# Kernel optimization log

Measured on AMD Instinct MI355X. Metric: run time of the kernel, lower is better.

Reference implementation:

```python
import jax, jax.numpy as jnp
import numpy as np

ALPHA = 0.2  # LeakyReLU negative slope
NEG_INF = -1.0e12


def setup_inputs() -> dict:
    key = jax.random.key(0)
    ks = jax.random.split(key, 8)
    N, F, D, H, M, Q = 4096, 512, 64, 4, 2, 128
    x = jax.random.normal(ks[0], (N, F), dtype=jnp.float32)
    adj = jax.random.randint(ks[1], (M, N, N), 0, 2, dtype=jnp.int32)
    W = jax.random.normal(ks[2], (H, F, D), dtype=jnp.float32) * 0.07
    a1 = jax.random.normal(ks[3], (H, D), dtype=jnp.float32) * 0.15
    a2 = jax.random.normal(ks[4], (H, D), dtype=jnp.float32) * 0.15
    Ws = jax.random.normal(ks[5], (H * D, Q), dtype=jnp.float32) * 0.1
    bs = jax.random.normal(ks[6], (1, Q), dtype=jnp.float32) * 0.1
    q_sem = jax.random.normal(ks[7], (Q, 1), dtype=jnp.float32) * 0.15
    return {"x": x, "adj": adj, "W": W, "a1": a1, "a2": a2,
            "Ws": Ws, "bs": bs, "q_sem": q_sem}


def reference(x, adj, W, a1, a2, Ws, bs, q_sem):
    N = x.shape[0]
    # Wh is identical across meta-paths (dropout disabled / eval mode)
    Wh = jnp.einsum('nf,hfd->hnd', x, W)            # [H,N,D]
    s1 = jnp.einsum('hnd,hd->hn', Wh, a1)           # Wh @ a[:D]
    s2 = jnp.einsum('hnd,hd->hn', Wh, a2)           # Wh @ a[D:]

    def metapath(adj_m):
        # e[h,i,j] = leaky_relu(s1[h,i] + s2[h,j]); mask by adjacency
        e = jax.nn.leaky_relu(s1[:, :, None] + s2[:, None, :], negative_slope=ALPHA)
        e = jnp.where(adj_m[None, :, :] > 0, e, NEG_INF)
        att = jax.nn.softmax(e, axis=2)             # softmax over neighbors (dim=1 in torch [N,N])
        h = jax.nn.elu(jnp.einsum('hnm,hmd->hnd', att, Wh))
        return jnp.transpose(h, (1, 0, 2)).reshape(N, -1)  # concat heads -> [N, H*D]

    Z = jax.vmap(metapath)(adj)                     # [M, N, H*D]
    z = jnp.transpose(Z, (1, 0, 2))                 # [N, M, H*D]

    # Semantic attention (faithful to original, incl. softmax over dim=1 of [M,1])
    Whs = jnp.tanh(jnp.einsum('nmf,fq->nmq', z, Ws) + bs)   # [N,M,Q]
    w = jnp.einsum('nmq,qo->nmo', Whs, q_sem).mean(0)        # [M,1]
    beta = jax.nn.softmax(w, axis=1)                          # [M,1]
    return (beta[None, :, :] * z).sum(axis=1)                 # [N, H*D]
```

## Files before the change

kernel.cpp:

```cpp
#include <hip/hip_runtime.h>
#include <hip/hip_fp16.h>
#include <stdint.h>

#define NN 4096
#define FF 512
#define DD 64
#define HH 4
#define MM 2
#define LOG2E 1.44269504088896340736f
#define ALPHA_LR 0.2f

typedef float f32x4 __attribute__((ext_vector_type(4)));
typedef _Float16 f16x8 __attribute__((ext_vector_type(8)));
typedef _Float16 f16x2 __attribute__((ext_vector_type(2)));
typedef unsigned short u16x2 __attribute__((ext_vector_type(2)));

extern "C" __device__ _Float16 __ocml_exp2_f16(_Float16);

union H4 { ushort4 u; _Float16 h[4]; };
union W8 { f16x8 v; uint32_t w[4]; f16x2 p[4]; };

__device__ inline float fast_exp2(float x) { return __builtin_amdgcn_exp2f(x); }
__device__ inline float fast_rcp(float x) { return __builtin_amdgcn_rcpf(x); }
__device__ inline f32x4 mfma16(f16x8 a, f16x8 b, f32x4 c) {
    return __builtin_amdgcn_mfma_f32_16x16x32_f16(a, b, c, 0, 0, 0);
}
__device__ inline uint32_t enc_f32(float f) {
    uint32_t u = __float_as_uint(f);
    return (u & 0x80000000u) ? ~u : (u | 0x80000000u);
}
__device__ inline float dec_f32(uint32_t k) {
    uint32_t u = (k & 0x80000000u) ? (k ^ 0x80000000u) : ~k;
    return __uint_as_float(u);
}
__device__ inline f16x2 msk01(uint32_t V, int k) {
    uint32_t w = (V >> (2 * k)) & 0x00010001u;
    u16x2 m = __builtin_bit_cast(u16x2, w) * (u16x2){0x3C00, 0x3C00};
    return __builtin_bit_cast(f16x2, m);
}
__device__ inline f16x2 pkmax(f16x2 a, f16x2 b) {
#if __has_builtin(__builtin_elementwise_max)
    return __builtin_elementwise_max(a, b);
#else
    return (f16x2){a[0] > b[0] ? a[0] : b[0], a[1] > b[1] ? a[1] : b[1]};
#endif
}

__global__ __launch_bounds__(256) void k_prep(const float* __restrict__ x,
                                              const int* __restrict__ adj,
                                              const float* __restrict__ W,
                                              _Float16* __restrict__ xh,
                                              _Float16* __restrict__ wt,
                                              unsigned long long* __restrict__ bitsT,
                                              uint32_t* __restrict__ m4a) {
    const int bid = blockIdx.x;
    if (bid < 2048) {
        const long long total = (long long)MM * NN * NN;
        const long long stride = 2048LL * 256;
        long long tid = (long long)bid * 256 + threadIdx.x;
        for (long long e = tid; e < total; e += stride) {
            unsigned long long msk = __ballot(adj[e] != 0);
            if ((threadIdx.x & 63) == 0) {
                long long q = e >> 6;
                int m  = (int)(q >> 18);
                int rem = (int)(q & 262143);
                int i  = rem >> 6;
                int jw = rem & 63;
                bitsT[((size_t)m * 64 + jw) * NN + i] = msk;
            }
        }
    } else if (bid < 4096) {
        int t = (bid - 2048) * 256 + threadIdx.x;
        if (t < HH) m4a[t] = 0u;
        float4 v = ((const float4*)x)[t];
        H4 o;
        o.h[0] = (_Float16)v.x; o.h[1] = (_Float16)v.y;
        o.h[2] = (_Float16)v.z; o.h[3] = (_Float16)v.w;
        ((ushort4*)xh)[t] = o.u;
    } else {
        int t = (bid - 4096) * 256 + threadIdx.x;
        int c = t >> 9, f = t & 511;
        int h = c >> 6, d = c & 63;
        wt[t] = (_Float16)W[(h * FF + f) * DD + d];
    }
}

__global__ __launch_bounds__(512) void k_wh(const _Float16* __restrict__ xh,
                                            const _Float16* __restrict__ wt,
                                            const float* __restrict__ a1,
                                            const float* __restrict__ a2,
                                            _Float16* __restrict__ whT,
                                            float* __restrict__ s1L,
                                            _Float16* __restrict__ s2h,
                                            uint32_t* __restrict__ m4a) {
    __shared__ float sred[8][2][16];
    const int wave = threadIdx.x >> 6;
    const int h    = wave & 3;
    const int th   = wave >> 2;
    const int lane = threadIdx.x & 63;
    const int iL   = lane & 15;
    const int quad = lane >> 4;
    const int i0   = blockIdx.x * 16;

    f32x4 acc[2];
    acc[0] = (f32x4){0.f, 0.f, 0.f, 0.f};
    acc[1] = (f32x4){0.f, 0.f, 0.f, 0.f};

    const _Float16* arow  = xh + (size_t)(i0 + iL) * FF + quad * 8;
    const _Float16* bbase = wt + (size_t)(h * 64 + th * 32 + iL) * FF + quad * 8;

    for (int kc = 0; kc < FF; kc += 32) {
        f16x8 a = *(const f16x8*)(arow + kc);
        #pragma unroll
        for (int u = 0; u < 2; ++u) {
            f16x8 b = *(const f16x8*)(bbase + (size_t)(16 * u) * FF + kc);
            acc[u] = mfma16(a, b, acc[u]);
        }
    }
    #pragma unroll
    for (int u = 0; u < 2; ++u) {
        H4 o;
        #pragma unroll
        for (int r = 0; r < 4; ++r) o.h[r] = (_Float16)acc[u][r];
        *(ushort4*)(whT + (size_t)(h * 64 + th * 32 + 16 * u + iL) * NN + i0 + quad * 4) = o.u;
    }

    const float a1v0 = a1[h * 64 + th * 32 + iL];
    const float a1v1 = a1[h * 64 + th * 32 + 16 + iL];
    const float a2v0 = a2[h * 64 + th * 32 + iL];
    const float a2v1 = a2[h * 64 + th * 32 + 16 + iL];
    #pragma unroll
    for (int r = 0; r < 4; ++r) {
        float p1 = acc[0][r] * a1v0 + acc[1][r] * a1v1;
        float p2 = acc[0][r] * a2v0 + acc[1][r] * a2v1;
        #pragma unroll
        for (int off = 1; off < 16; off <<= 1) {
            p1 += __shfl_xor(p1, off);
            p2 += __shfl_xor(p2, off);
        }
        if (iL == 0) {
            sred[wave][0][quad * 4 + r] = p1;
            sred[wave][1][quad * 4 + r] = p2;
        }
    }
    __syncthreads();
    if (threadIdx.x < 64) {
        int h2  = threadIdx.x >> 4;
        int idx = threadIdx.x & 15;
        float s1 = sred[h2][0][idx] + sred[h2 + 4][0][idx];
        float s2 = sred[h2][1][idx] + sred[h2 + 4][1][idx];
        float s2l = s2 * LOG2E;
        s1L[h2 * NN + i0 + idx] = s1 * LOG2E;
        s2h[h2 * NN + i0 + idx] = (_Float16)s2l;
        float mx = s2l;
        #pragma unroll
        for (int off = 1; off < 16; off <<= 1) mx = fmaxf(mx, __shfl_xor(mx, off));
        if (idx == 0) atomicMax(m4a + h2, enc_f32(mx));
    }
}

__global__ __launch_bounds__(512, 2) void k_attn(const _Float16* __restrict__ whT,
                                                 const float* __restrict__ s1L,
                                                 const _Float16* __restrict__ s2h,
                                                 const uint32_t* __restrict__ m4a,
                                                 const unsigned long long* __restrict__ bitsT,
                                                 float* __restrict__ out) {
    __shared__ __align__(16) float xr[8][MM][4][16][16];
    __shared__ __align__(16) float dr[8][MM][16];

    const int tid  = threadIdx.x;
    const int wave = tid >> 6;
    const int lane = tid & 63;
    const int iL   = lane & 15;
    const int quad = lane >> 4;
    const int h    = blockIdx.x & 3;
    const int i0   = (blockIdx.x >> 2) * 64;

    const float m4 = dec_f32(m4a[h]);
    f16x2 A2[4], B2[4];
    #pragma unroll
    for (int s = 0; s < 4; ++s) {
        float s1i = s1L[h * NN + i0 + 16 * s + iL];
        float vv  = s1i + m4;
        float cii = fmaxf(vv, ALPHA_LR * vv);
        _Float16 a = (_Float16)(s1i - cii);
        _Float16 b = (_Float16)(ALPHA_LR * s1i - cii);
        A2[s] = (f16x2){a, a};
        B2[s] = (f16x2){b, b};
    }
    const f16x2 al2 = (f16x2){(_Float16)ALPHA_LR, (_Float16)ALPHA_LR};

    f32x4 acc[4][MM][4];
    f32x4 accD[4][MM];
    #pragma unroll
    for (int s = 0; s < 4; ++s)
        #pragma unroll
        for (int m = 0; m < MM; ++m) {
            accD[s][m] = (f32x4){0.f, 0.f, 0.f, 0.f};
            #pragma unroll
            for (int t = 0; t < 4; ++t) acc[s][m][t] = (f32x4){0.f, 0.f, 0.f, 0.f};
        }

    f16x8 bones;
    #pragma unroll
    for (int e = 0; e < 8; ++e) bones[e] = (_Float16)1.0f;

    const _Float16* s2row = s2h + h * NN;
    const _Float16* brow = whT + (size_t)(h * 64 + iL) * NN;
    const int qshift = quad * 8;
    const int jbase = wave * 512;

    const unsigned long long* pB[MM][4];
    #pragma unroll
    for (int m = 0; m < MM; ++m)
        #pragma unroll
        for (int s = 0; s < 4; ++s)
            pB[m][s] = bitsT + (size_t)m * 64 * NN + i0 + 16 * s + iL;

    for (int it = 0; it < 8; ++it) {
        const int jc = jbase + it * 64;
        const int jw = jc >> 6;
        unsigned long long bm[MM][4];
        #pragma unroll
        for (int m = 0; m < MM; ++m)
            #pragma unroll
            for (int s = 0; s < 4; ++s)
                bm[m][s] = pB[m][s][(size_t)jw * NN];

        #pragma unroll
        for (int half = 0; half < 2; ++half) {
            const int jb = jc + 32 * half;
            f16x8 bfr[4];
            #pragma unroll
            for (int t = 0; t < 4; ++t)
                bfr[t] = *(const f16x8*)(brow + (size_t)(16 * t) * NN + jb + qshift);

            const W8 s2v = *(const W8*)(s2row + jb + qshift);
            const int shft = 32 * half + qshift;

            #pragma unroll
            for (int s = 0; s < 4; ++s) {
                uint32_t rs0 = (uint32_t)(bm[0][s] >> shft) & 0xFFu;
                uint32_t rs1 = (uint32_t)(bm[1][s] >> shft) & 0xFFu;
                uint32_t V0 = rs0 | (rs0 << 15);
                uint32_t V1 = rs1 | (rs1 << 15);
                W8 a0, a1v;
                #pragma unroll
                for (int k = 0; k < 4; ++k) {
                    f16x2 z = s2v.p[k] + A2[s];
                    f16x2 l = al2 * s2v.p[k] + B2[s];
                    f16x2 mx = pkmax(z, l);
                    f16x2 p = (f16x2){__ocml_exp2_f16(mx[0]), __ocml_exp2_f16(mx[1])};
                    a0.p[k]  = p * msk01(V0, k);
                    a1v.p[k] = p * msk01(V1, k);
                }
                #pragma unroll
                for (int t = 0; t < 4; ++t) {
                    acc[s][0][t] = mfma16(a0.v, bfr[t], acc[s][0][t]);
                    acc[s][1][t] = mfma16(a1v.v, bfr[t], acc[s][1][t]);
                }
                accD[s][0] = mfma16(a0.v, bones, accD[s][0]);
                accD[s][1] = mfma16(a1v.v, bones, accD[s][1]);
            }
        }
    }

    for (int s = 0; s < 4; ++s) {
        __syncthreads();
        #pragma unroll
        for (int m = 0; m < MM; ++m) {
            #pragma unroll
            for (int t = 0; t < 4; ++t)
                *(f32x4*)&xr[wave][m][t][iL][quad * 4] = acc[s][m][t];
            if (iL == 0) *(f32x4*)&dr[wave][m][quad * 4] = accD[s][m];
        }
        __syncthreads();
        if (wave < 4) {
            const int t = wave;
            f32x4 n0 = (f32x4){0.f, 0.f, 0.f, 0.f};
            f32x4 n1 = (f32x4){0.f, 0.f, 0.f, 0.f};
            f32x4 d0 = (f32x4){0.f, 0.f, 0.f, 0.f};
            f32x4 d1 = (f32x4){0.f, 0.f, 0.f, 0.f};
            #pragma unroll
            for (int sl = 0; sl < 8; ++sl) {
                n0 += *(const f32x4*)&xr[sl][0][t][iL][quad * 4];
                n1 += *(const f32x4*)&xr[sl][1][t][iL][quad * 4];
                d0 += *(const f32x4*)&dr[sl][0][quad * 4];
                d1 += *(const f32x4*)&dr[sl][1][quad * 4];
            }
            const int i0s = i0 + 16 * s;
            #pragma unroll
            for (int r = 0; r < 4; ++r) {
                float v0 = n0[r] * fast_rcp(d0[r]);
                float v1 = n1[r] * fast_rcp(d1[r]);
                float e0 = v0 > 0.f ? v0 : (fast_exp2(v0 * LOG2E) - 1.f);
                float e1 = v1 > 0.f ? v1 : (fast_exp2(v1 * LOG2E) - 1.f);
                out[(size_t)(i0s + quad * 4 + r) * (HH * DD) + h * 64 + 16 * t + iL] = e0 + e1;
            }
        }
    }
}

extern "C" void kernel_launch(void* const* d_in, const int* in_sizes, int n_in,
                              void* d_out, int out_size, void* d_ws, size_t ws_size,
                              hipStream_t stream) {
    const float* x   = (const float*)d_in[0];
    const int*   adj = (const int*)d_in[1];
    const float* W   = (const float*)d_in[2];
    const float* a1  = (const float*)d_in[3];
    const float* a2  = (const float*)d_in[4];
    float* out = (float*)d_out;

    char* ws = (char*)d_ws;
    _Float16* xh   = (_Float16*)(ws);
    _Float16* wt   = (_Float16*)(ws + 4194304);
    _Float16* whT  = (_Float16*)(ws + 4456448);
    float*    s1L  = (float*)(ws + 6553600);
    _Float16* s2h  = (_Float16*)(ws + 6619136);
    uint32_t* m4a  = (uint32_t*)(ws + 6684672);
    unsigned long long* bitsT = (unsigned long long*)(ws + 6750208);

    hipLaunchKernelGGL(k_prep, dim3(4608), dim3(256), 0, stream,
                       x, adj, W, xh, wt, bitsT, m4a);
    hipLaunchKernelGGL(k_wh, dim3(256), dim3(512), 0, stream,
                       xh, wt, a1, a2, whT, s1L, s2h, m4a);
    hipLaunchKernelGGL(k_attn, dim3(256), dim3(512), 0, stream,
                       whT, s1L, s2h, m4a, bitsT, out);
}
```

Before: 266.2 us.

## Restructure adjacency bit-packing, fuse x fp16 conversion into Wh GEMM, prefetch mask words

The adjacency packing now gives each block a 512-row by 64-column tile. Each wave issues 16 independent loads before its ballots, stages the masks in shared memory and writes them out as coalesced 128-bit stores, replacing scattered 8-byte stores. The separate x-to-fp16 conversion pass and its workspace buffer are removed; k_wh reads fp32 x directly and converts in registers. The attention kernel double-buffers the bitmask loads so the next iteration's mask words are fetched while the current one computes. The main risks are higher register pressure and the fp32 x being re-read by several blocks in k_wh.

```diff
diff --git a/kernel.cpp b/kernel.cpp
--- a/kernel.cpp
+++ b/kernel.cpp
@@ -46,46 +46,51 @@
 #endif
 }
 
-__global__ __launch_bounds__(256) void k_prep(const float* __restrict__ x,
-                                              const int* __restrict__ adj,
+__global__ __launch_bounds__(256) void k_prep(const int* __restrict__ adj,
                                               const float* __restrict__ W,
-                                              _Float16* __restrict__ xh,
                                               _Float16* __restrict__ wt,
                                               unsigned long long* __restrict__ bitsT,
                                               uint32_t* __restrict__ m4a) {
     const int bid = blockIdx.x;
-    if (bid < 2048) {
-        const long long total = (long long)MM * NN * NN;
-        const long long stride = 2048LL * 256;
-        long long tid = (long long)bid * 256 + threadIdx.x;
-        for (long long e = tid; e < total; e += stride) {
-            unsigned long long msk = __ballot(adj[e] != 0);
-            if ((threadIdx.x & 63) == 0) {
-                long long q = e >> 6;
-                int m  = (int)(q >> 18);
-                int rem = (int)(q & 262143);
-                int i  = rem >> 6;
-                int jw = rem & 63;
-                bitsT[((size_t)m * 64 + jw) * NN + i] = msk;
+    if (bid < 1024) {
+        __shared__ unsigned long long sw[512];
+        const int iq = bid & 7;
+        const int jw = (bid >> 3) & 63;
+        const int m  = bid >> 9;
+        const int w  = threadIdx.x >> 6;
+        const int l  = threadIdx.x & 63;
+        const int i0 = iq << 9;
+        const int* rp = adj + ((size_t)m << 24) + ((size_t)(i0 + (w << 7)) << 12)
+                        + (jw << 6) + l;
+        for (int t0 = 0; t0 < 128; t0 += 16) {
+            int v[16];
+            #pragma unroll
+            for (int u = 0; u < 16; ++u) v[u] = rp[(size_t)(t0 + u) << 12];
+            #pragma unroll
+            for (int u = 0; u < 16; ++u) {
+                unsigned long long msk = __ballot(v[u] != 0);
+                if (l == 0) sw[(w << 7) + t0 + u] = msk;
             }
         }
-    } else if (bid < 4096) {
-        int t = (bid - 2048) * 256 + threadIdx.x;
+        __syncthreads();
+        {
+            const int k = threadIdx.x;
+            unsigned long long* dst = bitsT + (((size_t)m * 64 + jw) << 12) + i0 + 2 * k;
+            ulonglong2 val;
+            val.x = sw[2 * k];
+            val.y = sw[2 * k + 1];
+            *(ulonglong2*)dst = val;
+        }
+    } else {
+        int t = (bid - 1024) * 256 + threadIdx.x;
         if (t < HH) m4a[t] = 0u;
-        float4 v = ((const float4*)x)[t];
-        H4 o;
-        o.h[0] = (_Float16)v.x; o.h[1] = (_Float16)v.y;
-        o.h[2] = (_Float16)v.z; o.h[3] = (_Float16)v.w;
-        ((ushort4*)xh)[t] = o.u;
-    } else {
-        int t = (bid - 4096) * 256 + threadIdx.x;
         int c = t >> 9, f = t & 511;
         int h = c >> 6, d = c & 63;
         wt[t] = (_Float16)W[(h * FF + f) * DD + d];
     }
 }
 
-__global__ __launch_bounds__(512) void k_wh(const _Float16* __restrict__ xh,
+__global__ __launch_bounds__(512) void k_wh(const float* __restrict__ x,
                                             const _Float16* __restrict__ wt,
                                             const float* __restrict__ a1,
                                             const float* __restrict__ a2,
@@ -106,11 +111,18 @@
     acc[0] = (f32x4){0.f, 0.f, 0.f, 0.f};
     acc[1] = (f32x4){0.f, 0.f, 0.f, 0.f};
 
-    const _Float16* arow  = xh + (size_t)(i0 + iL) * FF + quad * 8;
+    const float* arow = x + (size_t)(i0 + iL) * FF + quad * 8;
     const _Float16* bbase = wt + (size_t)(h * 64 + th * 32 + iL) * FF + quad * 8;
 
     for (int kc = 0; kc < FF; kc += 32) {
-        f16x8 a = *(const f16x8*)(arow + kc);
+        f32x4 xa = *(const f32x4*)(arow + kc);
+        f32x4 xb = *(const f32x4*)(arow + kc + 4);
+        f16x8 a;
+        #pragma unroll
+        for (int r = 0; r < 4; ++r) {
+            a[r]     = (_Float16)xa[r];
+            a[4 + r] = (_Float16)xb[r];
+        }
         #pragma unroll
         for (int u = 0; u < 2; ++u) {
             f16x8 b = *(const f16x8*)(bbase + (size_t)(16 * u) * FF + kc);
@@ -217,16 +229,17 @@
         for (int s = 0; s < 4; ++s)
             pB[m][s] = bitsT + (size_t)m * 64 * NN + i0 + 16 * s + iL;
 
-    for (int it = 0; it < 8; ++it) {
-        const int jc = jbase + it * 64;
-        const int jw = jc >> 6;
-        unsigned long long bm[MM][4];
+    auto loadB = [&](unsigned long long (&bm)[MM][4], int it) {
+        const int jw = (jbase + it * 64) >> 6;
         #pragma unroll
         for (int m = 0; m < MM; ++m)
             #pragma unroll
             for (int s = 0; s < 4; ++s)
                 bm[m][s] = pB[m][s][(size_t)jw * NN];
-
+    };
+
+    auto proc = [&](const unsigned long long (&bm)[MM][4], int it) {
+        const int jc = jbase + it * 64;
         #pragma unroll
         for (int half = 0; half < 2; ++half) {
             const int jb = jc + 32 * half;
@@ -263,6 +276,16 @@
                 accD[s][1] = mfma16(a1v.v, bones, accD[s][1]);
             }
         }
+    };
+
+    unsigned long long bmA[MM][4], bmB[MM][4];
+    loadB(bmA, 0);
+    #pragma unroll 1
+    for (int it = 0; it < 8; it += 2) {
+        loadB(bmB, it + 1);
+        proc(bmA, it);
+        if (it + 2 < 8) loadB(bmA, it + 2);
+        proc(bmB, it + 1);
     }
 
     for (int s = 0; s < 4; ++s) {
@@ -312,18 +335,17 @@
     float* out = (float*)d_out;
 
     char* ws = (char*)d_ws;
-    _Float16* xh   = (_Float16*)(ws);
-    _Float16* wt   = (_Float16*)(ws + 4194304);
-    _Float16* whT  = (_Float16*)(ws + 4456448);
-    float*    s1L  = (float*)(ws + 6553600);
-    _Float16* s2h  = (_Float16*)(ws + 6619136);
-    uint32_t* m4a  = (uint32_t*)(ws + 6684672);
-    unsigned long long* bitsT = (unsigned long long*)(ws + 6750208);
-
-    hipLaunchKernelGGL(k_prep, dim3(4608), dim3(256), 0, stream,
-                       x, adj, W, xh, wt, bitsT, m4a);
+    _Float16* wt   = (_Float16*)(ws);
+    _Float16* whT  = (_Float16*)(ws + 262144);
+    float*    s1L  = (float*)(ws + 2359296);
+    _Float16* s2h  = (_Float16*)(ws + 2424832);
+    uint32_t* m4a  = (uint32_t*)(ws + 2457600);
+    unsigned long long* bitsT = (unsigned long long*)(ws + 2490368);
+
+    hipLaunchKernelGGL(k_prep, dim3(1536), dim3(256), 0, stream,
+                       adj, W, wt, bitsT, m4a);
     hipLaunchKernelGGL(k_wh, dim3(256), dim3(512), 0, stream,
-                       xh, wt, a1, a2, whT, s1L, s2h, m4a);
+                       x, wt, a1, a2, whT, s1L, s2h, m4a);
     hipLaunchKernelGGL(k_attn, dim3(256), dim3(512), 0, stream,
                        whT, s1L, s2h, m4a, bitsT, out);
 }
```

New measurement: 299.7 us. +12.5%, slower.
